# Performance work log

Hardware: AMD Instinct MI355X
Metric: run time of the kernel (lower is better)

## Reference

```python
import jax, jax.numpy as jnp
import numpy as np

B = 2            # batch size
N_PRE = 50000    # presynaptic neurons
N_POST = 50000   # postsynaptic neurons
N_SYN = 10_000_000   # synapses (avg in-degree 200)
N_TYPES = 20     # synapse/receptor types (rows of basis table)
N_BASIS = 5      # receptor basis functions
SPIKE_P = 0.02   # spike probability per neuron per step


def setup_inputs() -> dict:
    key = jax.random.key(0)
    k1, k2, k3, k4, k5 = jax.random.split(key, 5)
    # binary spike buffer, like rec_z_buf (values in {0,1})
    rec_z_buf = (jax.random.uniform(k1, (B, N_PRE)) < SPIKE_P).astype(jnp.float32)
    weight_values = jax.random.normal(k2, (N_SYN,), dtype=jnp.float32) * 0.1
    synaptic_basis_weights = jax.random.uniform(k3, (N_TYPES, N_BASIS), dtype=jnp.float32)
    # col 0 = postsynaptic index, col 1 = presynaptic index
    synapse_indices = jax.random.randint(k4, (N_SYN, 2), 0, N_POST, dtype=jnp.int32)
    syn_ids = jax.random.randint(k5, (N_SYN,), 0, N_TYPES, dtype=jnp.int32)
    return {
        'rec_z_buf': rec_z_buf,
        'weight_values': weight_values,
        'synaptic_basis_weights': synaptic_basis_weights,
        'synapse_indices': synapse_indices,
        'syn_ids': syn_ids,
        'n_post': N_POST,
    }


def reference(rec_z_buf, weight_values, synaptic_basis_weights, synapse_indices, syn_ids, n_post):
    """I[b, post, r] = sum_syn spike[b, pre_syn] * W_syn * basis[syn_id_syn, r].

    Equivalent to the TF custom op: since spikes are binary, gating by
    spike > 0 equals multiplying by the spike value.
    Returns flat [B * n_post, n_basis] like i_rec_flat.
    """
    post = synapse_indices[:, 0]            # [n_syn]
    pre = synapse_indices[:, 1]             # [n_syn]
    # per-synapse weighted basis contribution [n_syn, R]
    contrib = weight_values[:, None] * synaptic_basis_weights[syn_ids]
    gathered = rec_z_buf[:, pre]            # [B, n_syn] spike gate per synapse
    per_syn = gathered[:, :, None] * contrib[None, :, :]   # [B, n_syn, R]
    # scatter-add into postsynaptic neurons, per batch element
    i_rec = jax.vmap(lambda x: jax.ops.segment_sum(x, post, num_segments=n_post))(per_syn)
    return i_rec.reshape(-1, i_rec.shape[-1])   # [B * n_post, R]
```

## Files before the change

### kernel.cpp

```cpp
#include <hip/hip_runtime.h>

#define N_PRE_C   50000
#define N_TYPES_C 20
#define N_BASIS_C 5
#define NB        2
#define WORDS     784

typedef unsigned long long ull;

__global__ __launch_bounds__(256) void pack_spikes(const float* __restrict__ rec_z,
                                                   ull* __restrict__ mask) {
    const int b = blockIdx.y;
    const int i = blockIdx.x * 256 + threadIdx.x;
    float v = 0.f;
    if (i < N_PRE_C) v = rec_z[b * N_PRE_C + i];
    ull m = __ballot(v > 0.f);
    if ((threadIdx.x & 63) == 0) mask[(i >> 6) * NB + b] = m;
}

__device__ __forceinline__ void proc_t(int post, int pre, float wv, int tt,
                                       const ull (*sm)[2],
                                       float* __restrict__ out_t, int n_post) {
    const int word = pre >> 6;
    const ull m0 = sm[word][0];
    const ull m1 = sm[word][1];
    const ull bit = 1ull << (pre & 63);
    if (((m0 | m1) & bit) == 0ull) return;
    if (m0 & bit) unsafeAtomicAdd(out_t + (long)post * N_TYPES_C + tt, wv);
    if (m1 & bit) unsafeAtomicAdd(out_t + (long)(n_post + post) * N_TYPES_C + tt, wv);
}

__global__ __launch_bounds__(256) void syn_scatter_t(
    const int4*  __restrict__ idx2,
    const float4* __restrict__ w4,
    const int4*  __restrict__ sid4,
    const ull*   __restrict__ mask,
    float* __restrict__ out_t,
    int n_post, int n_syn) {
    __shared__ __align__(16) ull sm[WORDS][2];
    {
        const ulonglong2* msrc = (const ulonglong2*)mask;
        ulonglong2* mdst = (ulonglong2*)sm;
        for (int t = threadIdx.x; t < WORDS; t += 256) mdst[t] = msrc[t];
    }
    __syncthreads();

    const int t = blockIdx.x * 256 + threadIdx.x;
    const long base = (long)t * 4;
    if (base >= n_syn) return;

    if (base + 4 <= n_syn) {
        const int4   p01 = idx2[(long)t * 2];
        const int4   p23 = idx2[(long)t * 2 + 1];
        const float4 wv  = w4[t];
        const int4   sv  = sid4[t];
        proc_t(p01.x, p01.y, wv.x, sv.x, sm, out_t, n_post);
        proc_t(p01.z, p01.w, wv.y, sv.y, sm, out_t, n_post);
        proc_t(p23.x, p23.y, wv.z, sv.z, sm, out_t, n_post);
        proc_t(p23.z, p23.w, wv.w, sv.w, sm, out_t, n_post);
    } else {
        const int*   idx = (const int*)idx2;
        const float* w   = (const float*)w4;
        const int*   sid = (const int*)sid4;
        for (long s = base; s < n_syn; ++s)
            proc_t(idx[2 * s], idx[2 * s + 1], w[s], sid[s], sm, out_t, n_post);
    }
}

__global__ __launch_bounds__(256) void combine_basis(
    const float* __restrict__ out_t,
    const float* __restrict__ basis,
    float* __restrict__ out, int rows) {
    __shared__ float sb[N_TYPES_C * N_BASIS_C];
    if (threadIdx.x < N_TYPES_C * N_BASIS_C) sb[threadIdx.x] = basis[threadIdx.x];
    __syncthreads();

    const int r = blockIdx.x * 256 + threadIdx.x;
    if (r >= rows) return;
    const float4* p = (const float4*)(out_t + (long)r * N_TYPES_C);
    float4 v0 = p[0], v1 = p[1], v2 = p[2], v3 = p[3], v4 = p[4];
    float vt[N_TYPES_C] = {v0.x, v0.y, v0.z, v0.w, v1.x, v1.y, v1.z, v1.w,
                           v2.x, v2.y, v2.z, v2.w, v3.x, v3.y, v3.z, v3.w,
                           v4.x, v4.y, v4.z, v4.w};
    float acc[N_BASIS_C] = {0.f, 0.f, 0.f, 0.f, 0.f};
    #pragma unroll
    for (int t = 0; t < N_TYPES_C; ++t) {
        #pragma unroll
        for (int k = 0; k < N_BASIS_C; ++k)
            acc[k] += vt[t] * sb[t * N_BASIS_C + k];
    }
    float* o = out + (long)r * N_BASIS_C;
    #pragma unroll
    for (int k = 0; k < N_BASIS_C; ++k) o[k] = acc[k];
}

__device__ __forceinline__ void proc_direct(int post, int pre, float wv, int tt,
                                            const ull (*sm)[2],
                                            const float (*sb)[N_BASIS_C],
                                            float* __restrict__ out, int n_post) {
    const int word = pre >> 6;
    const ull m0 = sm[word][0], m1 = sm[word][1];
    const ull bit = 1ull << (pre & 63);
    if (((m0 | m1) & bit) == 0ull) return;
    const float* bs = sb[tt];
    float c[N_BASIS_C];
    #pragma unroll
    for (int k = 0; k < N_BASIS_C; ++k) c[k] = wv * bs[k];
    if (m0 & bit) {
        float* o = out + (long)post * N_BASIS_C;
        #pragma unroll
        for (int k = 0; k < N_BASIS_C; ++k) unsafeAtomicAdd(o + k, c[k]);
    }
    if (m1 & bit) {
        float* o = out + (long)(n_post + post) * N_BASIS_C;
        #pragma unroll
        for (int k = 0; k < N_BASIS_C; ++k) unsafeAtomicAdd(o + k, c[k]);
    }
}

__global__ __launch_bounds__(256) void syn_scatter_direct(
    const int4* __restrict__ idx2, const float4* __restrict__ w4,
    const int4* __restrict__ sid4, const float* __restrict__ basis,
    const ull* __restrict__ mask, float* __restrict__ out,
    int n_post, int n_syn) {
    __shared__ __align__(16) ull sm[WORDS][2];
    __shared__ float sb[N_TYPES_C][N_BASIS_C];
    for (int t = threadIdx.x; t < WORDS * 2; t += 256) ((ull*)sm)[t] = mask[t];
    for (int t = threadIdx.x; t < N_TYPES_C * N_BASIS_C; t += 256)
        ((float*)sb)[t] = basis[t];
    __syncthreads();
    const int t = blockIdx.x * 256 + threadIdx.x;
    const long base = (long)t * 4;
    if (base >= n_syn) return;
    if (base + 4 <= n_syn) {
        const int4   p01 = idx2[(long)t * 2];
        const int4   p23 = idx2[(long)t * 2 + 1];
        const float4 wv  = w4[t];
        const int4   sv  = sid4[t];
        proc_direct(p01.x, p01.y, wv.x, sv.x, sm, sb, out, n_post);
        proc_direct(p01.z, p01.w, wv.y, sv.y, sm, sb, out, n_post);
        proc_direct(p23.x, p23.y, wv.z, sv.z, sm, sb, out, n_post);
        proc_direct(p23.z, p23.w, wv.w, sv.w, sm, sb, out, n_post);
    } else {
        const int*   idx = (const int*)idx2;
        const float* w   = (const float*)w4;
        const int*   sid = (const int*)sid4;
        for (long s = base; s < n_syn; ++s)
            proc_direct(idx[2 * s], idx[2 * s + 1], w[s], sid[s], sm, sb, out, n_post);
    }
}

extern "C" void kernel_launch(void* const* d_in, const int* in_sizes, int n_in,
                              void* d_out, int out_size, void* d_ws, size_t ws_size,
                              hipStream_t stream) {
    const float* rec_z   = (const float*)d_in[0];
    const float* weights = (const float*)d_in[1];
    const float* basis   = (const float*)d_in[2];
    const int*   synidx  = (const int*)d_in[3];
    const int*   synids  = (const int*)d_in[4];
    float*       out     = (float*)d_out;

    const int n_syn  = in_sizes[4];
    const int rows   = out_size / N_BASIS_C;
    const int n_post = rows / NB;
    const int n_thr  = (n_syn + 3) / 4;
    const int blocks = (n_thr + 255) / 256;

    const size_t out_t_bytes = (size_t)rows * N_TYPES_C * sizeof(float);
    const size_t mask_bytes  = (size_t)WORDS * NB * sizeof(ull);

    if (ws_size >= out_t_bytes + mask_bytes) {
        float* out_t = (float*)d_ws;
        ull*   mask  = (ull*)((char*)d_ws + out_t_bytes);

        hipMemsetAsync(out_t, 0, out_t_bytes, stream);
        pack_spikes<<<dim3(WORDS * 64 / 256, NB), 256, 0, stream>>>(rec_z, mask);
        syn_scatter_t<<<blocks, 256, 0, stream>>>(
            (const int4*)synidx, (const float4*)weights, (const int4*)synids,
            mask, out_t, n_post, n_syn);
        combine_basis<<<(rows + 255) / 256, 256, 0, stream>>>(out_t, basis, out, rows);
    } else {
        ull* mask = (ull*)d_ws;
        hipMemsetAsync(d_out, 0, (size_t)out_size * sizeof(float), stream);
        pack_spikes<<<dim3(WORDS * 64 / 256, NB), 256, 0, stream>>>(rec_z, mask);
        syn_scatter_direct<<<blocks, 256, 0, stream>>>(
            (const int4*)synidx, (const float4*)weights, (const int4*)synids,
            basis, mask, out, n_post, n_syn);
    }
}
```

Baseline: 195.9 us.

## Use persistent grid-stride scatter with software prefetch and fold zeroing into pack kernel

```diff
diff --git a/kernel.cpp b/kernel.cpp
--- a/kernel.cpp
+++ b/kernel.cpp
@@ -5,29 +5,36 @@
 #define N_BASIS_C 5
 #define NB        2
 #define WORDS     784
+#define SCAT_BLOCKS 2048
 
 typedef unsigned long long ull;
 
 __global__ __launch_bounds__(256) void pack_spikes(const float* __restrict__ rec_z,
-                                                   ull* __restrict__ mask) {
+                                                   ull* __restrict__ mask,
+                                                   float4* __restrict__ zbuf,
+                                                   int zquads) {
     const int b = blockIdx.y;
     const int i = blockIdx.x * 256 + threadIdx.x;
     float v = 0.f;
     if (i < N_PRE_C) v = rec_z[b * N_PRE_C + i];
-    ull m = __ballot(v > 0.f);
+    const ull m = __ballot(v > 0.f);
     if ((threadIdx.x & 63) == 0) mask[(i >> 6) * NB + b] = m;
-}
-
-__device__ __forceinline__ void proc_t(int post, int pre, float wv, int tt,
-                                       const ull (*sm)[2],
+
+    if (zbuf != nullptr) {
+        const int nt = gridDim.x * gridDim.y * 256;
+        int q = (blockIdx.y * gridDim.x + blockIdx.x) * 256 + threadIdx.x;
+        const float4 z = make_float4(0.f, 0.f, 0.f, 0.f);
+        for (; q < zquads; q += nt) zbuf[q] = z;
+    }
+}
+
+__device__ __forceinline__ void proc_m(int post, float wv, int tt, ull bit,
+                                       ulonglong2 mw,
                                        float* __restrict__ out_t, int n_post) {
-    const int word = pre >> 6;
-    const ull m0 = sm[word][0];
-    const ull m1 = sm[word][1];
-    const ull bit = 1ull << (pre & 63);
-    if (((m0 | m1) & bit) == 0ull) return;
-    if (m0 & bit) unsafeAtomicAdd(out_t + (long)post * N_TYPES_C + tt, wv);
-    if (m1 & bit) unsafeAtomicAdd(out_t + (long)(n_post + post) * N_TYPES_C + tt, wv);
+    if (((mw.x | mw.y) & bit) == 0ull) return;
+    const int o = post * N_TYPES_C + tt;
+    if (mw.x & bit) unsafeAtomicAdd(out_t + o, wv);
+    if (mw.y & bit) unsafeAtomicAdd(out_t + n_post * N_TYPES_C + o, wv);
 }
 
 __global__ __launch_bounds__(256) void syn_scatter_t(
@@ -44,26 +51,49 @@
         for (int t = threadIdx.x; t < WORDS; t += 256) mdst[t] = msrc[t];
     }
     __syncthreads();
-
-    const int t = blockIdx.x * 256 + threadIdx.x;
-    const long base = (long)t * 4;
-    if (base >= n_syn) return;
-
-    if (base + 4 <= n_syn) {
-        const int4   p01 = idx2[(long)t * 2];
-        const int4   p23 = idx2[(long)t * 2 + 1];
-        const float4 wv  = w4[t];
-        const int4   sv  = sid4[t];
-        proc_t(p01.x, p01.y, wv.x, sv.x, sm, out_t, n_post);
-        proc_t(p01.z, p01.w, wv.y, sv.y, sm, out_t, n_post);
-        proc_t(p23.x, p23.y, wv.z, sv.z, sm, out_t, n_post);
-        proc_t(p23.z, p23.w, wv.w, sv.w, sm, out_t, n_post);
-    } else {
+    const ulonglong2* sm2 = (const ulonglong2*)sm;
+
+    const int nq = n_syn >> 2;
+    const int stride = gridDim.x * 256;
+    int t = blockIdx.x * 256 + threadIdx.x;
+
+    if (t < nq) {
+        int4 p01 = idx2[(long)t * 2];
+        int4 p23 = idx2[(long)t * 2 + 1];
+        float4 wv = w4[t];
+        int4 sv   = sid4[t];
+        for (;;) {
+            const int tn = t + stride;
+            const bool vn = (tn < nq);
+            int4 q01, q23, qs; float4 qw;
+            if (vn) {
+                q01 = idx2[(long)tn * 2];
+                q23 = idx2[(long)tn * 2 + 1];
+                qw  = w4[tn];
+                qs  = sid4[tn];
+            }
+            const ulonglong2 m0 = sm2[p01.y >> 6];
+            const ulonglong2 m1 = sm2[p01.w >> 6];
+            const ulonglong2 m2 = sm2[p23.y >> 6];
+            const ulonglong2 m3 = sm2[p23.w >> 6];
+            proc_m(p01.x, wv.x, sv.x, 1ull << (p01.y & 63), m0, out_t, n_post);
+            proc_m(p01.z, wv.y, sv.y, 1ull << (p01.w & 63), m1, out_t, n_post);
+            proc_m(p23.x, wv.z, sv.z, 1ull << (p23.y & 63), m2, out_t, n_post);
+            proc_m(p23.z, wv.w, sv.w, 1ull << (p23.w & 63), m3, out_t, n_post);
+            if (!vn) break;
+            t = tn; p01 = q01; p23 = q23; wv = qw; sv = qs;
+        }
+    }
+
+    const int rem = n_syn & 3;
+    if (blockIdx.x == 0 && threadIdx.x < rem) {
+        const int s = (n_syn & ~3) + threadIdx.x;
         const int*   idx = (const int*)idx2;
         const float* w   = (const float*)w4;
         const int*   sid = (const int*)sid4;
-        for (long s = base; s < n_syn; ++s)
-            proc_t(idx[2 * s], idx[2 * s + 1], w[s], sid[s], sm, out_t, n_post);
+        const int post = idx[2 * s], pre = idx[2 * s + 1];
+        proc_m(post, w[s], sid[s], 1ull << (pre & 63), sm2[pre >> 6],
+               out_t, n_post);
     }
 }
 
@@ -163,8 +193,6 @@
     const int n_syn  = in_sizes[4];
     const int rows   = out_size / N_BASIS_C;
     const int n_post = rows / NB;
-    const int n_thr  = (n_syn + 3) / 4;
-    const int blocks = (n_thr + 255) / 256;
 
     const size_t out_t_bytes = (size_t)rows * N_TYPES_C * sizeof(float);
     const size_t mask_bytes  = (size_t)WORDS * NB * sizeof(ull);
@@ -173,16 +201,27 @@
         float* out_t = (float*)d_ws;
         ull*   mask  = (ull*)((char*)d_ws + out_t_bytes);
 
-        hipMemsetAsync(out_t, 0, out_t_bytes, stream);
-        pack_spikes<<<dim3(WORDS * 64 / 256, NB), 256, 0, stream>>>(rec_z, mask);
+        const int zquads = (int)(out_t_bytes / sizeof(float4));
+
+        pack_spikes<<<dim3(WORDS * 64 / 256, NB), 256, 0, stream>>>(
+            rec_z, mask, (float4*)out_t, zquads);
+
+        int blocks = SCAT_BLOCKS;
+        const int nq   = n_syn >> 2;
+        const int maxb = (nq + 255) / 256;
+        if (blocks > maxb) blocks = maxb;
+        if (blocks < 1)    blocks = 1;
         syn_scatter_t<<<blocks, 256, 0, stream>>>(
             (const int4*)synidx, (const float4*)weights, (const int4*)synids,
             mask, out_t, n_post, n_syn);
+
         combine_basis<<<(rows + 255) / 256, 256, 0, stream>>>(out_t, basis, out, rows);
     } else {
         ull* mask = (ull*)d_ws;
         hipMemsetAsync(d_out, 0, (size_t)out_size * sizeof(float), stream);
-        pack_spikes<<<dim3(WORDS * 64 / 256, NB), 256, 0, stream>>>(rec_z, mask);
+        pack_spikes<<<dim3(WORDS * 64 / 256, NB), 256, 0, stream>>>(
+            rec_z, mask, nullptr, 0);
+        const int blocks = ((n_syn + 3) / 4 + 255) / 256;
         syn_scatter_direct<<<blocks, 256, 0, stream>>>(
             (const int4*)synidx, (const float4*)weights, (const int4*)synids,
             basis, mask, out, n_post, n_syn);
```

After: 197.1 us. About the same (+0.6%).

## Compact active synapses into a list before applying weights and types

Applied to the files above, without the earlier changes.

```diff
diff --git a/kernel.cpp b/kernel.cpp
--- a/kernel.cpp
+++ b/kernel.cpp
@@ -5,65 +5,118 @@
 #define N_BASIS_C 5
 #define NB        2
 #define WORDS     784
+#define BCAP      1024
 
 typedef unsigned long long ull;
 
 __global__ __launch_bounds__(256) void pack_spikes(const float* __restrict__ rec_z,
-                                                   ull* __restrict__ mask) {
+                                                   ull* __restrict__ mask,
+                                                   float4* __restrict__ zbuf,
+                                                   int zquads,
+                                                   int* __restrict__ cnt) {
     const int b = blockIdx.y;
     const int i = blockIdx.x * 256 + threadIdx.x;
     float v = 0.f;
     if (i < N_PRE_C) v = rec_z[b * N_PRE_C + i];
-    ull m = __ballot(v > 0.f);
+    const ull m = __ballot(v > 0.f);
     if ((threadIdx.x & 63) == 0) mask[(i >> 6) * NB + b] = m;
-}
-
-__device__ __forceinline__ void proc_t(int post, int pre, float wv, int tt,
-                                       const ull (*sm)[2],
-                                       float* __restrict__ out_t, int n_post) {
-    const int word = pre >> 6;
-    const ull m0 = sm[word][0];
-    const ull m1 = sm[word][1];
-    const ull bit = 1ull << (pre & 63);
-    if (((m0 | m1) & bit) == 0ull) return;
-    if (m0 & bit) unsafeAtomicAdd(out_t + (long)post * N_TYPES_C + tt, wv);
-    if (m1 & bit) unsafeAtomicAdd(out_t + (long)(n_post + post) * N_TYPES_C + tt, wv);
-}
-
-__global__ __launch_bounds__(256) void syn_scatter_t(
-    const int4*  __restrict__ idx2,
-    const float4* __restrict__ w4,
-    const int4*  __restrict__ sid4,
-    const ull*   __restrict__ mask,
+    if (cnt != nullptr && b == 0 && i == 0) *cnt = 0;
+
+    if (zbuf != nullptr) {
+        const int nt = gridDim.x * gridDim.y * 256;
+        int q = (blockIdx.y * gridDim.x + blockIdx.x) * 256 + threadIdx.x;
+        const float4 z = make_float4(0.f, 0.f, 0.f, 0.f);
+        for (; q < zquads; q += nt) zbuf[q] = z;
+    }
+}
+
+__device__ __forceinline__ void push_e(unsigned dst20, unsigned s,
+                                       uint2* __restrict__ buf, int* __restrict__ bcnt,
+                                       uint2* __restrict__ list, int* __restrict__ cnt,
+                                       int cap,
+                                       const float* __restrict__ w,
+                                       const int* __restrict__ sid,
+                                       float* __restrict__ out_t) {
+    const int slot = atomicAdd(bcnt, 1);
+    if (slot < BCAP) { buf[slot] = make_uint2(dst20, s); return; }
+    const int g = atomicAdd(cnt, 1);
+    if (g < cap) { list[g] = make_uint2(dst20, s); return; }
+    unsafeAtomicAdd(out_t + dst20 + sid[s], w[s]);
+}
+
+__global__ __launch_bounds__(256) void syn_compact(
+    const int4* __restrict__ idx4,
+    const ull*  __restrict__ mask,
+    uint2* __restrict__ list, int* __restrict__ cnt, int cap,
+    const float* __restrict__ w, const int* __restrict__ sid,
     float* __restrict__ out_t,
     int n_post, int n_syn) {
     __shared__ __align__(16) ull sm[WORDS][2];
+    __shared__ __align__(16) uint2 buf[BCAP];
+    __shared__ int bcnt, gbase;
     {
         const ulonglong2* msrc = (const ulonglong2*)mask;
         ulonglong2* mdst = (ulonglong2*)sm;
         for (int t = threadIdx.x; t < WORDS; t += 256) mdst[t] = msrc[t];
     }
-    __syncthreads();
-
-    const int t = blockIdx.x * 256 + threadIdx.x;
-    const long base = (long)t * 4;
-    if (base >= n_syn) return;
-
-    if (base + 4 <= n_syn) {
-        const int4   p01 = idx2[(long)t * 2];
-        const int4   p23 = idx2[(long)t * 2 + 1];
-        const float4 wv  = w4[t];
-        const int4   sv  = sid4[t];
-        proc_t(p01.x, p01.y, wv.x, sv.x, sm, out_t, n_post);
-        proc_t(p01.z, p01.w, wv.y, sv.y, sm, out_t, n_post);
-        proc_t(p23.x, p23.y, wv.z, sv.z, sm, out_t, n_post);
-        proc_t(p23.z, p23.w, wv.w, sv.w, sm, out_t, n_post);
-    } else {
-        const int*   idx = (const int*)idx2;
-        const float* w   = (const float*)w4;
-        const int*   sid = (const int*)sid4;
-        for (long s = base; s < n_syn; ++s)
-            proc_t(idx[2 * s], idx[2 * s + 1], w[s], sid[s], sm, out_t, n_post);
+    if (threadIdx.x == 0) bcnt = 0;
+    __syncthreads();
+    const ulonglong2* sm2 = (const ulonglong2*)sm;
+    const unsigned np20 = (unsigned)n_post * N_TYPES_C;
+
+    auto proc = [&](int post, int pre, unsigned s) {
+        const ulonglong2 mw = sm2[pre >> 6];
+        const ull bit = 1ull << (pre & 63);
+        if (((mw.x | mw.y) & bit) == 0ull) return;
+        const unsigned d20 = (unsigned)post * N_TYPES_C;
+        if (mw.x & bit) push_e(d20, s, buf, &bcnt, list, cnt, cap, w, sid, out_t);
+        if (mw.y & bit) push_e(d20 + np20, s, buf, &bcnt, list, cnt, cap, w, sid, out_t);
+    };
+
+    const int gt = blockIdx.x * 256 + threadIdx.x;
+    const long s0 = (long)gt * 8;
+    if (s0 < n_syn) {
+        if (s0 + 8 <= n_syn) {
+            const int4 a = idx4[gt * 4 + 0];
+            const int4 b = idx4[gt * 4 + 1];
+            const int4 c = idx4[gt * 4 + 2];
+            const int4 d = idx4[gt * 4 + 3];
+            const unsigned u = (unsigned)s0;
+            proc(a.x, a.y, u + 0); proc(a.z, a.w, u + 1);
+            proc(b.x, b.y, u + 2); proc(b.z, b.w, u + 3);
+            proc(c.x, c.y, u + 4); proc(c.z, c.w, u + 5);
+            proc(d.x, d.y, u + 6); proc(d.z, d.w, u + 7);
+        } else {
+            const int2* p = (const int2*)idx4;
+            for (long s = s0; s < n_syn; ++s) {
+                const int2 e = p[s];
+                proc(e.x, e.y, (unsigned)s);
+            }
+        }
+    }
+
+    __syncthreads();
+    const int n = bcnt < BCAP ? bcnt : BCAP;
+    if (threadIdx.x == 0) gbase = atomicAdd(cnt, n);
+    __syncthreads();
+    for (int i = threadIdx.x; i < n; i += 256) {
+        const int g = gbase + i;
+        const uint2 e = buf[i];
+        if (g < cap) list[g] = e;
+        else unsafeAtomicAdd(out_t + e.x + sid[e.y], w[e.y]);
+    }
+}
+
+__global__ __launch_bounds__(256) void syn_apply(
+    const float* __restrict__ w, const int* __restrict__ sid,
+    const uint2* __restrict__ list, const int* __restrict__ cnt, int cap,
+    float* __restrict__ out_t) {
+    int n = *cnt;
+    if (n > cap) n = cap;
+    const int stride = gridDim.x * 256;
+    for (int i = blockIdx.x * 256 + threadIdx.x; i < n; i += stride) {
+        const uint2 e = list[i];
+        unsafeAtomicAdd(out_t + e.x + (unsigned)sid[e.y], w[e.y]);
     }
 }
 
@@ -163,26 +216,39 @@
     const int n_syn  = in_sizes[4];
     const int rows   = out_size / N_BASIS_C;
     const int n_post = rows / NB;
-    const int n_thr  = (n_syn + 3) / 4;
-    const int blocks = (n_thr + 255) / 256;
 
     const size_t out_t_bytes = (size_t)rows * N_TYPES_C * sizeof(float);
     const size_t mask_bytes  = (size_t)WORDS * NB * sizeof(ull);
-
-    if (ws_size >= out_t_bytes + mask_bytes) {
+    const size_t fixed_bytes = out_t_bytes + mask_bytes + 16;
+    const size_t want_list   = (size_t)(n_syn / 8 + 1024) * 8;
+
+    if (ws_size >= fixed_bytes + want_list) {
         float* out_t = (float*)d_ws;
         ull*   mask  = (ull*)((char*)d_ws + out_t_bytes);
-
-        hipMemsetAsync(out_t, 0, out_t_bytes, stream);
-        pack_spikes<<<dim3(WORDS * 64 / 256, NB), 256, 0, stream>>>(rec_z, mask);
-        syn_scatter_t<<<blocks, 256, 0, stream>>>(
-            (const int4*)synidx, (const float4*)weights, (const int4*)synids,
-            mask, out_t, n_post, n_syn);
+        int*   cnt   = (int*)((char*)d_ws + out_t_bytes + mask_bytes);
+        uint2* list  = (uint2*)((char*)d_ws + fixed_bytes);
+        const size_t cap_sz = (ws_size - fixed_bytes) / sizeof(uint2);
+        const int cap = cap_sz > 0x7ffffff0ull ? 0x7ffffff0 : (int)cap_sz;
+
+        const int zquads = (int)(out_t_bytes / sizeof(float4));
+        pack_spikes<<<dim3(WORDS * 64 / 256, NB), 256, 0, stream>>>(
+            rec_z, mask, (float4*)out_t, zquads, cnt);
+
+        const int n_thr  = (n_syn + 7) / 8;
+        const int blocks = (n_thr + 255) / 256;
+        syn_compact<<<blocks, 256, 0, stream>>>(
+            (const int4*)synidx, mask, list, cnt, cap,
+            weights, synids, out_t, n_post, n_syn);
+
+        syn_apply<<<2048, 256, 0, stream>>>(weights, synids, list, cnt, cap, out_t);
+
         combine_basis<<<(rows + 255) / 256, 256, 0, stream>>>(out_t, basis, out, rows);
     } else {
         ull* mask = (ull*)d_ws;
         hipMemsetAsync(d_out, 0, (size_t)out_size * sizeof(float), stream);
-        pack_spikes<<<dim3(WORDS * 64 / 256, NB), 256, 0, stream>>>(rec_z, mask);
+        pack_spikes<<<dim3(WORDS * 64 / 256, NB), 256, 0, stream>>>(
+            rec_z, mask, nullptr, 0, nullptr);
+        const int blocks = ((n_syn + 3) / 4 + 255) / 256;
         syn_scatter_direct<<<blocks, 256, 0, stream>>>(
             (const int4*)synidx, (const float4*)weights, (const int4*)synids,
             basis, mask, out, n_post, n_syn);
```

New measurement: 245.0 us. 1.25x slower.

## Defer weight and type loads until a spike hits; fold zeroing into spike packing

Applied to the files above, without the earlier changes.

```diff
diff --git a/kernel.cpp b/kernel.cpp
--- a/kernel.cpp
+++ b/kernel.cpp
@@ -4,66 +4,106 @@
 #define N_TYPES_C 20
 #define N_BASIS_C 5
 #define NB        2
-#define WORDS     784
+#define WORDS32   1568
 
 typedef unsigned long long ull;
+typedef unsigned int uint_t;
 
 __global__ __launch_bounds__(256) void pack_spikes(const float* __restrict__ rec_z,
-                                                   ull* __restrict__ mask) {
+                                                   uint_t* __restrict__ mask32,
+                                                   float4* __restrict__ zbuf,
+                                                   int zquads) {
     const int b = blockIdx.y;
     const int i = blockIdx.x * 256 + threadIdx.x;
     float v = 0.f;
     if (i < N_PRE_C) v = rec_z[b * N_PRE_C + i];
-    ull m = __ballot(v > 0.f);
-    if ((threadIdx.x & 63) == 0) mask[(i >> 6) * NB + b] = m;
-}
-
-__device__ __forceinline__ void proc_t(int post, int pre, float wv, int tt,
-                                       const ull (*sm)[2],
-                                       float* __restrict__ out_t, int n_post) {
-    const int word = pre >> 6;
-    const ull m0 = sm[word][0];
-    const ull m1 = sm[word][1];
-    const ull bit = 1ull << (pre & 63);
-    if (((m0 | m1) & bit) == 0ull) return;
-    if (m0 & bit) unsafeAtomicAdd(out_t + (long)post * N_TYPES_C + tt, wv);
-    if (m1 & bit) unsafeAtomicAdd(out_t + (long)(n_post + post) * N_TYPES_C + tt, wv);
+    const ull m = __ballot(v > 0.f);
+    if ((threadIdx.x & 63) == 0) {
+        const int w32 = i >> 5;
+        mask32[(w32 + 0) * NB + b] = (uint_t)(m & 0xffffffffull);
+        mask32[(w32 + 1) * NB + b] = (uint_t)(m >> 32);
+    }
+
+    if (zbuf != nullptr) {
+        const int nt = gridDim.x * gridDim.y * 256;
+        int q = (blockIdx.y * gridDim.x + blockIdx.x) * 256 + threadIdx.x;
+        const float4 z = make_float4(0.f, 0.f, 0.f, 0.f);
+        for (; q < zquads; q += nt) zbuf[q] = z;
+    }
 }
 
 __global__ __launch_bounds__(256) void syn_scatter_t(
     const int4*  __restrict__ idx2,
     const float4* __restrict__ w4,
     const int4*  __restrict__ sid4,
-    const ull*   __restrict__ mask,
+    const uint2* __restrict__ mask2,
     float* __restrict__ out_t,
     int n_post, int n_syn) {
-    __shared__ __align__(16) ull sm[WORDS][2];
+    __shared__ __align__(16) uint2 sm[WORDS32];
     {
-        const ulonglong2* msrc = (const ulonglong2*)mask;
-        ulonglong2* mdst = (ulonglong2*)sm;
-        for (int t = threadIdx.x; t < WORDS; t += 256) mdst[t] = msrc[t];
+        const uint4* msrc = (const uint4*)mask2;
+        uint4* mdst = (uint4*)sm;
+        for (int t = threadIdx.x; t < WORDS32 / 2; t += 256) mdst[t] = msrc[t];
     }
     __syncthreads();
 
     const int t = blockIdx.x * 256 + threadIdx.x;
     const long base = (long)t * 4;
     if (base >= n_syn) return;
+    const int np20 = n_post * N_TYPES_C;
 
     if (base + 4 <= n_syn) {
-        const int4   p01 = idx2[(long)t * 2];
-        const int4   p23 = idx2[(long)t * 2 + 1];
-        const float4 wv  = w4[t];
-        const int4   sv  = sid4[t];
-        proc_t(p01.x, p01.y, wv.x, sv.x, sm, out_t, n_post);
-        proc_t(p01.z, p01.w, wv.y, sv.y, sm, out_t, n_post);
-        proc_t(p23.x, p23.y, wv.z, sv.z, sm, out_t, n_post);
-        proc_t(p23.z, p23.w, wv.w, sv.w, sm, out_t, n_post);
+        const int4 p01 = idx2[t * 2];
+        const int4 p23 = idx2[t * 2 + 1];
+        const uint2 m0 = sm[p01.y >> 5];
+        const uint2 m1 = sm[p01.w >> 5];
+        const uint2 m2 = sm[p23.y >> 5];
+        const uint2 m3 = sm[p23.w >> 5];
+        const uint_t b0 = 1u << (p01.y & 31);
+        const uint_t b1 = 1u << (p01.w & 31);
+        const uint_t b2 = 1u << (p23.y & 31);
+        const uint_t b3 = 1u << (p23.w & 31);
+        const uint_t f0 = (m0.x | m0.y) & b0;
+        const uint_t f1 = (m1.x | m1.y) & b1;
+        const uint_t f2 = (m2.x | m2.y) & b2;
+        const uint_t f3 = (m3.x | m3.y) & b3;
+        if (f0 | f1 | f2 | f3) {
+            const float4 wv = w4[t];
+            const int4   sv = sid4[t];
+            if (f0) {
+                const int o = p01.x * N_TYPES_C + sv.x;
+                if (m0.x & b0) unsafeAtomicAdd(out_t + o, wv.x);
+                if (m0.y & b0) unsafeAtomicAdd(out_t + o + np20, wv.x);
+            }
+            if (f1) {
+                const int o = p01.z * N_TYPES_C + sv.y;
+                if (m1.x & b1) unsafeAtomicAdd(out_t + o, wv.y);
+                if (m1.y & b1) unsafeAtomicAdd(out_t + o + np20, wv.y);
+            }
+            if (f2) {
+                const int o = p23.x * N_TYPES_C + sv.z;
+                if (m2.x & b2) unsafeAtomicAdd(out_t + o, wv.z);
+                if (m2.y & b2) unsafeAtomicAdd(out_t + o + np20, wv.z);
+            }
+            if (f3) {
+                const int o = p23.z * N_TYPES_C + sv.w;
+                if (m3.x & b3) unsafeAtomicAdd(out_t + o, wv.w);
+                if (m3.y & b3) unsafeAtomicAdd(out_t + o + np20, wv.w);
+            }
+        }
     } else {
         const int*   idx = (const int*)idx2;
         const float* w   = (const float*)w4;
         const int*   sid = (const int*)sid4;
-        for (long s = base; s < n_syn; ++s)
-            proc_t(idx[2 * s], idx[2 * s + 1], w[s], sid[s], sm, out_t, n_post);
+        for (long s = base; s < n_syn; ++s) {
+            const int post = idx[2 * s], pre = idx[2 * s + 1];
+            const uint2 mw = sm[pre >> 5];
+            const uint_t bit = 1u << (pre & 31);
+            if (((mw.x | mw.y) & bit) == 0u) continue;
+            const int o = post * N_TYPES_C + sid[s];
+            if (mw.x & bit) unsafeAtomicAdd(out_t + o, w[s]);
+            if (mw.y & bit) unsafeAtomicAdd(out_t + o + np20, w[s]);
+        }
     }
 }
 
@@ -94,59 +134,56 @@
     for (int k = 0; k < N_BASIS_C; ++k) o[k] = acc[k];
 }
 
-__device__ __forceinline__ void proc_direct(int post, int pre, float wv, int tt,
-                                            const ull (*sm)[2],
-                                            const float (*sb)[N_BASIS_C],
-                                            float* __restrict__ out, int n_post) {
-    const int word = pre >> 6;
-    const ull m0 = sm[word][0], m1 = sm[word][1];
-    const ull bit = 1ull << (pre & 63);
-    if (((m0 | m1) & bit) == 0ull) return;
-    const float* bs = sb[tt];
-    float c[N_BASIS_C];
-    #pragma unroll
-    for (int k = 0; k < N_BASIS_C; ++k) c[k] = wv * bs[k];
-    if (m0 & bit) {
-        float* o = out + (long)post * N_BASIS_C;
-        #pragma unroll
-        for (int k = 0; k < N_BASIS_C; ++k) unsafeAtomicAdd(o + k, c[k]);
-    }
-    if (m1 & bit) {
-        float* o = out + (long)(n_post + post) * N_BASIS_C;
-        #pragma unroll
-        for (int k = 0; k < N_BASIS_C; ++k) unsafeAtomicAdd(o + k, c[k]);
-    }
-}
-
 __global__ __launch_bounds__(256) void syn_scatter_direct(
     const int4* __restrict__ idx2, const float4* __restrict__ w4,
     const int4* __restrict__ sid4, const float* __restrict__ basis,
-    const ull* __restrict__ mask, float* __restrict__ out,
+    const uint2* __restrict__ mask2, float* __restrict__ out,
     int n_post, int n_syn) {
-    __shared__ __align__(16) ull sm[WORDS][2];
+    __shared__ __align__(16) uint2 sm[WORDS32];
     __shared__ float sb[N_TYPES_C][N_BASIS_C];
-    for (int t = threadIdx.x; t < WORDS * 2; t += 256) ((ull*)sm)[t] = mask[t];
+    for (int t = threadIdx.x; t < WORDS32; t += 256) sm[t] = mask2[t];
     for (int t = threadIdx.x; t < N_TYPES_C * N_BASIS_C; t += 256)
         ((float*)sb)[t] = basis[t];
     __syncthreads();
     const int t = blockIdx.x * 256 + threadIdx.x;
     const long base = (long)t * 4;
     if (base >= n_syn) return;
+
+    auto apply = [&](int post, int pre, float wv, int tt) {
+        const uint2 mw = sm[pre >> 5];
+        const uint_t bit = 1u << (pre & 31);
+        if (((mw.x | mw.y) & bit) == 0u) return;
+        const float* bs = sb[tt];
+        float c[N_BASIS_C];
+        #pragma unroll
+        for (int k = 0; k < N_BASIS_C; ++k) c[k] = wv * bs[k];
+        if (mw.x & bit) {
+            float* o = out + (long)post * N_BASIS_C;
+            #pragma unroll
+            for (int k = 0; k < N_BASIS_C; ++k) unsafeAtomicAdd(o + k, c[k]);
+        }
+        if (mw.y & bit) {
+            float* o = out + (long)(n_post + post) * N_BASIS_C;
+            #pragma unroll
+            for (int k = 0; k < N_BASIS_C; ++k) unsafeAtomicAdd(o + k, c[k]);
+        }
+    };
+
     if (base + 4 <= n_syn) {
-        const int4   p01 = idx2[(long)t * 2];
-        const int4   p23 = idx2[(long)t * 2 + 1];
+        const int4   p01 = idx2[t * 2];
+        const int4   p23 = idx2[t * 2 + 1];
         const float4 wv  = w4[t];
         const int4   sv  = sid4[t];
-        proc_direct(p01.x, p01.y, wv.x, sv.x, sm, sb, out, n_post);
-        proc_direct(p01.z, p01.w, wv.y, sv.y, sm, sb, out, n_post);
-        proc_direct(p23.x, p23.y, wv.z, sv.z, sm, sb, out, n_post);
-        proc_direct(p23.z, p23.w, wv.w, sv.w, sm, sb, out, n_post);
+        apply(p01.x, p01.y, wv.x, sv.x);
+        apply(p01.z, p01.w, wv.y, sv.y);
+        apply(p23.x, p23.y, wv.z, sv.z);
+        apply(p23.z, p23.w, wv.w, sv.w);
     } else {
         const int*   idx = (const int*)idx2;
         const float* w   = (const float*)w4;
         const int*   sid = (const int*)sid4;
         for (long s = base; s < n_syn; ++s)
-            proc_direct(idx[2 * s], idx[2 * s + 1], w[s], sid[s], sm, sb, out, n_post);
+            apply(idx[2 * s], idx[2 * s + 1], w[s], sid[s]);
     }
 }
 
@@ -167,24 +204,28 @@
     const int blocks = (n_thr + 255) / 256;
 
     const size_t out_t_bytes = (size_t)rows * N_TYPES_C * sizeof(float);
-    const size_t mask_bytes  = (size_t)WORDS * NB * sizeof(ull);
+    const size_t mask_bytes  = (size_t)WORDS32 * NB * sizeof(uint_t);
 
     if (ws_size >= out_t_bytes + mask_bytes) {
-        float* out_t = (float*)d_ws;
-        ull*   mask  = (ull*)((char*)d_ws + out_t_bytes);
-
-        hipMemsetAsync(out_t, 0, out_t_bytes, stream);
-        pack_spikes<<<dim3(WORDS * 64 / 256, NB), 256, 0, stream>>>(rec_z, mask);
+        float*  out_t  = (float*)d_ws;
+        uint_t* mask32 = (uint_t*)((char*)d_ws + out_t_bytes);
+
+        const int zquads = (int)(out_t_bytes / sizeof(float4));
+        pack_spikes<<<dim3(WORDS32 * 32 / 256, NB), 256, 0, stream>>>(
+            rec_z, mask32, (float4*)out_t, zquads);
+
         syn_scatter_t<<<blocks, 256, 0, stream>>>(
             (const int4*)synidx, (const float4*)weights, (const int4*)synids,
-            mask, out_t, n_post, n_syn);
+            (const uint2*)mask32, out_t, n_post, n_syn);
+
         combine_basis<<<(rows + 255) / 256, 256, 0, stream>>>(out_t, basis, out, rows);
     } else {
-        ull* mask = (ull*)d_ws;
+        uint_t* mask32 = (uint_t*)d_ws;
         hipMemsetAsync(d_out, 0, (size_t)out_size * sizeof(float), stream);
-        pack_spikes<<<dim3(WORDS * 64 / 256, NB), 256, 0, stream>>>(rec_z, mask);
+        pack_spikes<<<dim3(WORDS32 * 32 / 256, NB), 256, 0, stream>>>(
+            rec_z, mask32, nullptr, 0);
         syn_scatter_direct<<<blocks, 256, 0, stream>>>(
             (const int4*)synidx, (const float4*)weights, (const int4*)synids,
-            basis, mask, out, n_post, n_syn);
-    }
-}
+            basis, (const uint2*)mask32, out, n_post, n_syn);
+    }
+}
```

After: 198.7 us. About the same (+1.4%).
